# Kernel optimization log

Hardware: AMD Instinct MI355X
Metric: run time of the kernel (lower is better)

The kernel has to match this reference:

```python
import jax, jax.numpy as jnp
import numpy as np
from jax import lax

B, S, F = 64, 63, 64          # batch, window length, num_past_features
T, NF, OUT = 12, 63, 1        # pred_sequence_length, forecast feats, output_size
C, K = 32, 3                  # hidden channels, kernel size
DILS = (1, 2, 4, 8, 16)       # S = (K-1)*sum(DILS)+1 = 63 -> conv stack reduces to length 1


def setup_inputs() -> dict:
    key = jax.random.key(0)
    ks = jax.random.split(key, 8)
    sc = 0.1
    x = jax.random.normal(ks[0], (B, S, F), dtype=jnp.float32)
    x_forecasts = jax.random.normal(ks[1], (B, T, NF), dtype=jnp.float32)
    # per-feature conv stacks stored as grouped-conv weights (feature_group_count=F)
    w0 = jax.random.normal(ks[2], (F * C, 1, K), dtype=jnp.float32) * sc
    b0 = jnp.zeros((F * C,), dtype=jnp.float32)
    wmid = jax.random.normal(ks[3], (3, F * C, C, K), dtype=jnp.float32) * sc
    bmid = jnp.zeros((3, F * C), dtype=jnp.float32)
    wlast = jax.random.normal(ks[4], (F * 1, C, K), dtype=jnp.float32) * sc
    blast = jnp.zeros((F,), dtype=jnp.float32)
    linW = jax.random.normal(ks[5], (OUT, F + NF), dtype=jnp.float32) * sc
    linb = jnp.zeros((OUT,), dtype=jnp.float32)
    return dict(x=x, x_forecasts=x_forecasts, w0=w0, b0=b0, wmid=wmid,
                bmid=bmid, wlast=wlast, blast=blast, linW=linW, linb=linb)


def _dconv(h, w, d):
    # h: [B, F*Cin, L]; grouped dilated conv, one group per past feature
    return lax.conv_general_dilated(h, w, window_strides=(1,), padding='VALID',
                                    rhs_dilation=(d,),
                                    dimension_numbers=('NCH', 'OIH', 'NCH'),
                                    feature_group_count=F)


def _step(xw, xf, w0, b0, wmid, bmid, wlast, blast, linW, linb):
    # xw: [B, S, F] window; xf: [B, NF] forecast features for this step
    h = jnp.transpose(xw, (0, 2, 1))                       # [B, F, S]
    h = jax.nn.relu(_dconv(h, w0, DILS[0]) + b0[None, :, None])
    for k in range(3):
        h = jax.nn.relu(_dconv(h, wmid[k], DILS[k + 1]) + bmid[k][None, :, None])
    h = _dconv(h, wlast, DILS[4]) + blast[None, :, None]   # [B, F, 1], no final relu
    feat = jnp.concatenate([h[:, :, 0], xf], axis=1)       # [B, F+NF]
    return feat @ linW.T + linb                            # [B, OUT]


def reference(x, x_forecasts, w0, b0, wmid, bmid, wlast, blast, linW, linb):
    params = (w0, b0, wmid, bmid, wlast, blast, linW, linb)
    out0 = _step(x, x_forecasts[:, 0], *params)

    def body(carry, xs):
        xw, prev = carry
        xf_i, xf_ip1 = xs
        add = jnp.concatenate([xf_i, prev], axis=1)[:, None, :]   # [B,1,F] since NF+OUT=F
        xw = jnp.concatenate([xw[:, 1:, :], add], axis=1)          # slide window
        out = _step(xw, xf_ip1, *params)
        return (xw, out), out

    xs = (jnp.swapaxes(x_forecasts[:, :-1], 0, 1),   # [T-1, B, NF]
          jnp.swapaxes(x_forecasts[:, 1:], 0, 1))
    _, outs = lax.scan(body, (x, out0), xs)          # [T-1, B, OUT]
    return jnp.swapaxes(jnp.concatenate([out0[None], outs], axis=0), 0, 1)  # [B, T, OUT]
```

## Files before the change

### kernel.cpp

```cpp
#include <hip/hip_runtime.h>


typedef _Float16 f16;
typedef _Float16 h2 __attribute__((ext_vector_type(2)));
typedef _Float16 f16x4 __attribute__((ext_vector_type(4)));
typedef _Float16 f16x8 __attribute__((ext_vector_type(8)));
typedef float f32x16 __attribute__((ext_vector_type(16)));

#define OFF_H4    0
#define OFF_ST    49152
#define ST_L0     0
#define ST_L1     128
#define ST_L2     384
#define ST_L3     896
#define ST_STRIDE 1760
#define OFF_H40   161792
#define OFF_RECH  161856
#define OFF_PRM   166464
#define OFF_XFT   167488

#define RECH_N 9216
#define TAIL_N 59392

#define RPAD 36
#define NROW 72

__device__ __forceinline__ void stage_wrow(
    const float* __restrict__ wmid, int m, int f, int tid, f16* wrow)
{
  const float* src = wmid + m * 196608 + f * 3072 + tid * 12;
  f16* dst = wrow + (tid >> 3) * 100 + (tid & 7) * 12;
#pragma unroll
  for (int u = 0; u < 3; ++u) {
    const float4 v = *reinterpret_cast<const float4*>(src + u * 4);
    dst[u * 4 + 0] = (f16)v.x; dst[u * 4 + 1] = (f16)v.y;
    dst[u * 4 + 2] = (f16)v.z; dst[u * 4 + 3] = (f16)v.w;
  }
}

__device__ __forceinline__ void mfma_tile2(
    const f16* IN, f16* OUT, int d, int base,
    const f16* __restrict__ wrow, int lane, const float* sBias)
{
  const int lg = lane >> 5;
  const int co = lane & 31;
  const int col = base + co;

  f16x8 afr[6];
#pragma unroll
  for (int h = 0; h < 2; ++h) {
    const f16* wp = wrow + co * 100 + (h * 16 + lg * 8) * 3;
    f16x4 w4[6];
#pragma unroll
    for (int u = 0; u < 6; ++u) w4[u] = *(const f16x4*)(wp + u * 4);
#pragma unroll
    for (int t = 0; t < 3; ++t)
#pragma unroll
      for (int j = 0; j < 8; ++j) {
        const int o = 3 * j + t;
        afr[t * 2 + h][j] = w4[o >> 2][o & 3];
      }
  }

  f32x16 acc;
#pragma unroll
  for (int r = 0; r < 16; ++r)
    acc[r] = sBias[(r & 3) + 8 * (r >> 2) + 4 * lg];

#pragma unroll
  for (int t = 0; t < 3; ++t) {
#pragma unroll
    for (int h = 0; h < 2; ++h) {
      const f16* bp = IN + (col + t * d) * RPAD + h * 16 + lg * 8;
      f16x4 lo = *(const f16x4*)bp;
      f16x4 hi = *(const f16x4*)(bp + 4);
      f16x8 b = __builtin_shufflevector(lo, hi, 0, 1, 2, 3, 4, 5, 6, 7);
      acc = __builtin_amdgcn_mfma_f32_32x32x16_f16(afr[t * 2 + h], b, acc, 0, 0, 0);
    }
  }

#pragma unroll
  for (int q = 0; q < 4; ++q) {
    const int co0 = q * 8 + 4 * lg;
    f16x4 w;
#pragma unroll
    for (int e = 0; e < 4; ++e)
      w[e] = (f16)fmaxf(acc[q * 4 + e], 0.f);
    *(f16x4*)(OUT + col * RPAD + co0) = w;
  }
}

__global__ __launch_bounds__(256) void tcn_pre(
    const float* __restrict__ x, const float* __restrict__ xfc,
    const float* __restrict__ w0, const float* __restrict__ b0,
    const float* __restrict__ wmid, const float* __restrict__ bmid,
    const float* __restrict__ wlast, const float* __restrict__ blast,
    const float* __restrict__ linW, const float* __restrict__ linb,
    float* __restrict__ ws)
{
  const int blk = blockIdx.x;
  const int tid = threadIdx.x;

  if (blk >= 4096) {
    const int idx = (blk - 4096) * 256 + tid;
    if (idx < RECH_N) {
      const int e = idx & 7, lane = (idx >> 3) & 63, q = idx >> 9;
      const int i = q * 8 + e;
      const int m = i / 48, r2 = i % 48;
      const int k = r2 >> 4, ci = r2 & 15;
      const int c = lane & 31, cib = (lane >> 5) * 16;
      ((f16*)(ws + OFF_RECH))[idx] =
          (f16)wmid[m * 196608 + (2016 + c) * 96 + (cib + ci) * 3 + k];
    } else if (idx < RECH_N + 1024) {
      const int r = idx - RECH_N;
      const int e = r & 3, lane = (r >> 2) & 63, q = r >> 8;
      const int i = q * 4 + e;
      const int c = lane & 31;
      float v = 0.f;
      if (i < 3)        v = w0[(2016 + c) * 3 + i];
      else if (i == 3)  v = b0[2016 + c];
      else if (i < 7)   v = bmid[(i - 4) * 2048 + 2016 + c];
      else if (i < 10)  v = wlast[63 * 96 + c * 3 + (i - 7)];
      else if (i == 10) v = blast[63];
      else if (i == 11) v = linW[63];
      else if (i == 12) v = linb[0];
      ws[OFF_PRM + r] = v;
    } else if (idx < TAIL_N) {
      const int r = idx - (RECH_N + 1024);
      const int b = r / 768, rem = r % 768;
      const int q = rem >> 8, lane = (rem >> 2) & 63, e = rem & 3;
      const int i = q * 4 + e;
      ws[OFF_XFT + r] = (lane < 63 && i < 12) ? xfc[(b * 12 + i) * 63 + lane] : 0.f;
    }
    return;
  }

  const int b = blk >> 6;
  const int f = blk & 63;
  const bool lastf = (f == 63);
  const int lane = tid & 63;
  const int g = __builtin_amdgcn_readfirstlane(tid >> 6);

  __shared__ float sIn[80];
  __shared__ float sBias[3][32];
  __shared__ f16 actA[NROW * RPAD];
  __shared__ f16 actB[NROW * RPAD];
  __shared__ __align__(8) f16 wrow[32 * 100];

  for (int t = tid; t < 80; t += 256) {
    float v = 0.f;
    if (t < 63)                 v = x[(b * 63 + t) * 64 + f];
    else if (t < 74 && !lastf)  v = xfc[(b * 12 + (t - 63)) * 63 + f];
    sIn[t] = v;
  }
  if (tid < 96) sBias[tid >> 5][tid & 31] = bmid[(tid >> 5) * 2048 + f * 32 + (tid & 31)];
  stage_wrow(wmid, 0, f, tid, wrow);
  __syncthreads();

  {
    const float* wb  = w0 + (f * 32 + g * 8) * 3;
    const float* bbp = b0 + f * 32 + g * 8;
#pragma unroll
    for (int it = 0; it < 2; ++it) {
      const int p = lane + it * 64;
      if (p < 72) {
        const float i0 = sIn[p], i1 = sIn[p + 1], i2 = sIn[p + 2];
        f16x4 wv[2];
#pragma unroll
        for (int j = 0; j < 8; ++j) {
          float v = fmaf(wb[j * 3 + 0], i0,
                    fmaf(wb[j * 3 + 1], i1,
                    fmaf(wb[j * 3 + 2], i2, bbp[j])));
          wv[j >> 2][j & 3] = (f16)fmaxf(v, 0.f);
        }
        *(f16x4*)(actA + p * RPAD + g * 8)     = wv[0];
        *(f16x4*)(actA + p * RPAD + g * 8 + 4) = wv[1];
      }
    }
  }
  __syncthreads();

  float* st = ws + OFF_ST + b * ST_STRIDE;

  if (lastf) {
    for (int t = tid; t < 128; t += 256)
      st[ST_L0 + t] = (float)actA[(57 + (t >> 5)) * RPAD + (t & 31)];
  }
  if (g < 3) mfma_tile2(actA, actB, 2, (g == 2) ? 36 : g * 32, wrow, lane, sBias[0]);
  __syncthreads();

  stage_wrow(wmid, 1, f, tid, wrow);
  if (lastf) {
    for (int t = tid; t < 256; t += 256)
      st[ST_L1 + t] = (float)actB[(49 + (t >> 5)) * RPAD + (t & 31)];
  }
  __syncthreads();

  if (g < 2) mfma_tile2(actB, actA, 4, g * 28, wrow, lane, sBias[1]);
  __syncthreads();

  stage_wrow(wmid, 2, f, tid, wrow);
  if (lastf) {
    for (int t = tid; t < 512; t += 256)
      st[ST_L2 + t] = (float)actA[(33 + (t >> 5)) * RPAD + (t & 31)];
  }
  __syncthreads();

  if (g < 2) mfma_tile2(actA, actB, 8, g * 12, wrow, lane, sBias[2]);
  __syncthreads();

  if (lastf) {
    for (int t = tid; t < 864; t += 256)
      st[ST_L3 + t] = (float)actB[(1 + (t >> 5)) * RPAD + (t & 31)];
  }
  if (tid < 12) {
    const int p = tid;
    float acc = blast[f];
    const float* wl = wlast + f * 96;
#pragma unroll
    for (int k = 0; k < 3; ++k) {
      const int row = p + 16 * k;
#pragma unroll
      for (int ci0 = 0; ci0 < 32; ci0 += 4) {
        f16x4 av = *(const f16x4*)(actB + row * RPAD + ci0);
#pragma unroll
        for (int e = 0; e < 4; ++e)
          acc = fmaf(wl[(ci0 + e) * 3 + k], (float)av[e], acc);
      }
    }
    if (!lastf) {
      ws[OFF_H4 + b * 768 + (p >> 2) * 256 + f * 4 + (p & 3)] = acc;
    } else {
      ws[OFF_H4 + b * 768 + (p >> 2) * 256 + 63 * 4 + (p & 3)] = 0.f;
      if (p == 0) ws[OFF_H40 + b] = acc;
    }
  }
}


__device__ __forceinline__ float fd2(h2 a, h2 b, float c) {
#if __has_builtin(__builtin_amdgcn_fdot2)
  return __builtin_amdgcn_fdot2(a, b, c, false);
#else
  return fmaf((float)a[0], (float)b[0], fmaf((float)a[1], (float)b[1], c));
#endif
}

__device__ __forceinline__ float dotv(f16x8 w, f16x8 a, float acc) {
  h2 w0 = {w[0], w[1]}, a0 = {a[0], a[1]};
  h2 w1 = {w[2], w[3]}, a1 = {a[2], a[3]};
  h2 w2 = {w[4], w[5]}, a2 = {a[4], a[5]};
  h2 w3 = {w[6], w[7]}, a3 = {a[6], a[7]};
  acc = fd2(w0, a0, acc);
  acc = fd2(w1, a1, acc);
  acc = fd2(w2, a2, acc);
  acc = fd2(w3, a3, acc);
  return acc;
}

__device__ __forceinline__ f16x8 combineh(f16x8 lo, f16x8 hi) {
  f16x8 s = lo + hi;
#pragma unroll
  for (int i = 0; i < 8; ++i) s[i] = (s[i] > (f16)0.f) ? s[i] : (f16)0.f;
  return s;
}

__device__ __forceinline__ void load16f(const float* p, float* r) {
  const float4* q = reinterpret_cast<const float4*>(p);
  const float4 v0 = q[0], v1 = q[1], v2 = q[2], v3 = q[3];
  r[0]=v0.x;  r[1]=v0.y;  r[2]=v0.z;  r[3]=v0.w;
  r[4]=v1.x;  r[5]=v1.y;  r[6]=v1.z;  r[7]=v1.w;
  r[8]=v2.x;  r[9]=v2.y;  r[10]=v2.z; r[11]=v2.w;
  r[12]=v3.x; r[13]=v3.y; r[14]=v3.z; r[15]=v3.w;
}

__global__ __launch_bounds__(256, 1) void tcn_seq(
    const float* __restrict__ x,
    const float* __restrict__ linW,
    const float* __restrict__ ws, float* __restrict__ out)
{
  const int b = blockIdx.x;
  const int tid = threadIdx.x;
  const int wid = tid >> 6;
  const int lane = tid & 63;
  const int c = lane & 31;
  const int h = (lane >> 5) & 1;
  const int cib = h * 16;

  __shared__ __align__(16) f16 L0h[15 * 32];
  __shared__ __align__(16) f16 L1p[2][19 * 32];
  __shared__ __align__(16) f16 L2p[2][27 * 32];
  __shared__ __align__(16) f16 wseqh[18 * 64 * 8];
  __shared__ __align__(16) float qs[32];
  __shared__ float preArr[12];

  const float* stp = ws + OFF_ST + b * ST_STRIDE;

  if (wid == 1) {
    const f16* rech = (const f16*)(ws + OFF_RECH);
#pragma unroll
    for (int q = 0; q < 18; ++q)
      *(f16x8*)(wseqh + (q * 64 + lane) * 8) = *(const f16x8*)(rech + (q * 64 + lane) * 8);
  } else if (wid == 2) {
    for (int t = lane; t < 128; t += 64) L0h[t] = (f16)stp[ST_L0 + t];
    for (int t = lane; t < 256; t += 64) { L1p[0][t] = (f16)stp[ST_L1 + t]; L1p[1][t] = (f16)0.f; }
  } else if (wid == 3) {
    for (int t = lane; t < 512; t += 64) { L2p[0][t] = (f16)stp[ST_L2 + t]; L2p[1][t] = (f16)0.f; }
  }
  if (wid != 0) { __syncthreads(); return; }

  float prm[16];
  {
    const float* tab = ws + OFF_PRM;
#pragma unroll
    for (int q = 0; q < 4; ++q) {
      const float4 v = *reinterpret_cast<const float4*>(tab + (q * 64 + lane) * 4);
      prm[q * 4 + 0] = v.x; prm[q * 4 + 1] = v.y;
      prm[q * 4 + 2] = v.z; prm[q * 4 + 3] = v.w;
    }
  }
  const float w00 = prm[0],  w01 = prm[1],  w02 = prm[2],  b00 = prm[3];
  const float bm0 = prm[4],  bm1 = prm[5],  bm2 = prm[6];
  const float wl0c = prm[7], wl1c = prm[8], wl2c = prm[9];
  const float bl = prm[10],  lw63 = prm[11], lb0 = prm[12];

  const float xv61 = x[(b * 63 + 61) * 64 + 63];
  const float xv62 = x[(b * 63 + 62) * 64 + 63];
  const float h40v = ws[OFF_H40 + b];

  float accv[12];
  {
    float lw = 0.f, lwx = 0.f;
    if (lane < 63) { lw = linW[lane]; lwx = linW[64 + lane]; }
    float h4v[12], xv[12];
#pragma unroll
    for (int q = 0; q < 3; ++q) {
      const float4 hv  = *reinterpret_cast<const float4*>(ws + OFF_H4 + b * 768 + q * 256 + lane * 4);
      const float4 xvv = *reinterpret_cast<const float4*>(ws + OFF_XFT + b * 768 + q * 256 + lane * 4);
      h4v[q*4+0] = hv.x; h4v[q*4+1] = hv.y; h4v[q*4+2] = hv.z; h4v[q*4+3] = hv.w;
      xv[q*4+0] = xvv.x; xv[q*4+1] = xvv.y; xv[q*4+2] = xvv.z; xv[q*4+3] = xvv.w;
    }
#pragma unroll
    for (int i = 0; i < 12; ++i) accv[i] = fmaf(lw, h4v[i], lwx * xv[i]);

    if (lane < 32) {
#pragma unroll
      for (int i = 1; i < 12; ++i) {
        const float qc = fmaf(wl0c, stp[ST_L3 + (i - 1) * 32 + lane],
                              wl1c * stp[ST_L3 + (i + 15) * 32 + lane]);
        accv[i] = fmaf(lw63, qc, accv[i]);
      }
    }
#pragma unroll
    for (int r = 1; r < 64; r <<= 1) {
#pragma unroll
      for (int i = 0; i < 12; ++i) accv[i] += __shfl_xor(accv[i], r);
    }
  }
  if (lane == 0) {
#pragma unroll
    for (int i = 1; i < 12; ++i) preArr[i] = accv[i] + lb0 + lw63 * bl;
  }
  __syncthreads();

  const f16* wbase = wseqh;
  asm volatile("" : "+v"(wbase));

  const float out0 = fmaf(lw63, h40v, accv[0] + lb0);
  if (lane == 0) out[b * 12 + 0] = out0;
  float o1 = out0, o2 = xv62, o3 = xv61;

#pragma unroll 1
  for (int s = 1; s < 12; ++s) {
    const float preS = preArr[s];

    const float nL0 = fmaxf(fmaf(w00, o3, fmaf(w01, o2, fmaf(w02, o1, b00))), 0.f);
    L0h[(3 + s) * 32 + c] = (f16)nL0;

    float v1;
    {
      const f16* wp = wbase + (0 * 6 * 64 + lane) * 8;
      f16x8 W0 = *(const f16x8*)(wp);
      f16x8 W1 = *(const f16x8*)(wp + 64 * 8);
      f16x8 W2 = *(const f16x8*)(wp + 2 * 64 * 8);
      f16x8 W3 = *(const f16x8*)(wp + 3 * 64 * 8);
      f16x8 W4 = *(const f16x8*)(wp + 4 * 64 * 8);
      f16x8 W5 = *(const f16x8*)(wp + 5 * 64 * 8);
      const f16* r0p = L0h + (s - 1) * 32 + cib;
      const f16* r1p = L0h + (s + 1) * 32 + cib;
      const f16* np  = L0h + (3 + s) * 32 + cib;
      f16x8 R0a = *(const f16x8*)r0p, R0b = *(const f16x8*)(r0p + 8);
      f16x8 R1a = *(const f16x8*)r1p, R1b = *(const f16x8*)(r1p + 8);
      f16x8 Na  = *(const f16x8*)np,  Nb  = *(const f16x8*)(np + 8);
      float a0 = dotv(W0, R0a, 0.f), a1 = dotv(W1, R0b, 0.f);
      a0 = dotv(W2, R1a, a0);        a1 = dotv(W3, R1b, a1);
      a0 = dotv(W4, Na, a0);         a1 = dotv(W5, Nb, a1);
      v1 = a0 + a1 + (h == 0 ? bm0 : 0.f);
    }
    L1p[h][(7 + s) * 32 + c] = (f16)v1;

    float v2;
    {
      const f16* wp = wbase + (1 * 6 * 64 + lane) * 8;
      f16x8 W0 = *(const f16x8*)(wp);
      f16x8 W1 = *(const f16x8*)(wp + 64 * 8);
      f16x8 W2 = *(const f16x8*)(wp + 2 * 64 * 8);
      f16x8 W3 = *(const f16x8*)(wp + 3 * 64 * 8);
      f16x8 W4 = *(const f16x8*)(wp + 4 * 64 * 8);
      f16x8 W5 = *(const f16x8*)(wp + 5 * 64 * 8);
      const int i0 = (s - 1) * 32 + cib, i1 = (s + 3) * 32 + cib, in = (7 + s) * 32 + cib;
      f16x8 R0a = combineh(*(const f16x8*)(&L1p[0][i0]),     *(const f16x8*)(&L1p[1][i0]));
      f16x8 R0b = combineh(*(const f16x8*)(&L1p[0][i0 + 8]), *(const f16x8*)(&L1p[1][i0 + 8]));
      f16x8 R1a = combineh(*(const f16x8*)(&L1p[0][i1]),     *(const f16x8*)(&L1p[1][i1]));
      f16x8 R1b = combineh(*(const f16x8*)(&L1p[0][i1 + 8]), *(const f16x8*)(&L1p[1][i1 + 8]));
      f16x8 Na  = combineh(*(const f16x8*)(&L1p[0][in]),     *(const f16x8*)(&L1p[1][in]));
      f16x8 Nb  = combineh(*(const f16x8*)(&L1p[0][in + 8]), *(const f16x8*)(&L1p[1][in + 8]));
      float a0 = dotv(W0, R0a, 0.f), a1 = dotv(W1, R0b, 0.f);
      a0 = dotv(W2, R1a, a0);        a1 = dotv(W3, R1b, a1);
      a0 = dotv(W4, Na, a0);         a1 = dotv(W5, Nb, a1);
      v2 = a0 + a1 + (h == 0 ? bm1 : 0.f);
    }
    L2p[h][(15 + s) * 32 + c] = (f16)v2;

    float v3;
    {
      const f16* wp = wbase + (2 * 6 * 64 + lane) * 8;
      f16x8 W0 = *(const f16x8*)(wp);
      f16x8 W1 = *(const f16x8*)(wp + 64 * 8);
      f16x8 W2 = *(const f16x8*)(wp + 2 * 64 * 8);
      f16x8 W3 = *(const f16x8*)(wp + 3 * 64 * 8);
      f16x8 W4 = *(const f16x8*)(wp + 4 * 64 * 8);
      f16x8 W5 = *(const f16x8*)(wp + 5 * 64 * 8);
      const int i0 = (s - 1) * 32 + cib, i1 = (s + 7) * 32 + cib, in = (15 + s) * 32 + cib;
      f16x8 R0a = combineh(*(const f16x8*)(&L2p[0][i0]),     *(const f16x8*)(&L2p[1][i0]));
      f16x8 R0b = combineh(*(const f16x8*)(&L2p[0][i0 + 8]), *(const f16x8*)(&L2p[1][i0 + 8]));
      f16x8 R1a = combineh(*(const f16x8*)(&L2p[0][i1]),     *(const f16x8*)(&L2p[1][i1]));
      f16x8 R1b = combineh(*(const f16x8*)(&L2p[0][i1 + 8]), *(const f16x8*)(&L2p[1][i1 + 8]));
      f16x8 Na  = combineh(*(const f16x8*)(&L2p[0][in]),     *(const f16x8*)(&L2p[1][in]));
      f16x8 Nb  = combineh(*(const f16x8*)(&L2p[0][in + 8]), *(const f16x8*)(&L2p[1][in + 8]));
      float a0 = dotv(W0, R0a, 0.f), a1 = dotv(W1, R0b, 0.f);
      a0 = dotv(W2, R1a, a0);        a1 = dotv(W3, R1b, a1);
      a0 = dotv(W4, Na, a0);         a1 = dotv(W5, Nb, a1);
      v3 = a0 + a1 + (h == 0 ? bm2 : 0.f);
    }
    v3 += __shfl_xor(v3, 32);
    const float nL3 = fmaxf(v3, 0.f);

    if (h == 0) qs[c] = wl2c * nL3;
    float qa[16], qb[16];
    load16f(qs, qa); load16f(qs + 16, qb);
    float s0 = 0.f, s1 = 0.f, s2 = 0.f, s3 = 0.f;
#pragma unroll
    for (int i = 0; i < 16; i += 4) {
      s0 += qa[i + 0] + qb[i + 0];
      s1 += qa[i + 1] + qb[i + 1];
      s2 += qa[i + 2] + qb[i + 2];
      s3 += qa[i + 3] + qb[i + 3];
    }
    const float S = (s0 + s1) + (s2 + s3);
    const float outs = fmaf(lw63, S, preS);
    if (lane == 0) out[b * 12 + s] = outs;
    o3 = o2; o2 = o1; o1 = outs;
  }
}


extern "C" void kernel_launch(void* const* d_in, const int* in_sizes, int n_in,
                              void* d_out, int out_size, void* d_ws, size_t ws_size,
                              hipStream_t stream) {
  const float* x     = (const float*)d_in[0];
  const float* xfc   = (const float*)d_in[1];
  const float* w0    = (const float*)d_in[2];
  const float* b0    = (const float*)d_in[3];
  const float* wmid  = (const float*)d_in[4];
  const float* bmid  = (const float*)d_in[5];
  const float* wlast = (const float*)d_in[6];
  const float* blast = (const float*)d_in[7];
  const float* linW  = (const float*)d_in[8];
  const float* linb  = (const float*)d_in[9];
  float* out = (float*)d_out;
  float* ws  = (float*)d_ws;

  tcn_pre<<<4096 + 232, 256, 0, stream>>>(
      x, xfc, w0, b0, wmid, bmid, wlast, blast, linW, linb, ws);
  tcn_seq<<<64, 256, 0, stream>>>(x, linW, ws, out);
}
```

Baseline: 37.15 us.

## Process two batch elements per block in tcn_pre to reuse staged weights

Each compute block now handles two batch samples for one feature, which halves the grid from 4096 to 2048 compute blocks. The staged mid-layer weights and biases are reused across both samples, and the MFMA tiles are spread so all four waves stay busy on the layers where only two or three were active before. This cuts redundant weight loads and conversions and improves wave utilisation, at the cost of doubled LDS for activations and fewer blocks to hide latency.

```diff
diff --git a/kernel.cpp b/kernel.cpp
--- a/kernel.cpp
+++ b/kernel.cpp
@@ -21,9 +21,11 @@
 
 #define RECH_N 9216
 #define TAIL_N 59392
+#define NCOMP  2048
 
 #define RPAD 36
 #define NROW 72
+#define ASZ  (NROW * RPAD)
 
 __device__ __forceinline__ void stage_wrow(
     const float* __restrict__ wmid, int m, int f, int tid, f16* wrow)
@@ -101,8 +103,8 @@
   const int blk = blockIdx.x;
   const int tid = threadIdx.x;
 
-  if (blk >= 4096) {
-    const int idx = (blk - 4096) * 256 + tid;
+  if (blk >= NCOMP) {
+    const int idx = (blk - NCOMP) * 256 + tid;
     if (idx < RECH_N) {
       const int e = idx & 7, lane = (idx >> 3) & 63, q = idx >> 9;
       const int i = q * 8 + e;
@@ -135,23 +137,25 @@
     return;
   }
 
-  const int b = blk >> 6;
+  const int bp = blk >> 6;
   const int f = blk & 63;
   const bool lastf = (f == 63);
   const int lane = tid & 63;
   const int g = __builtin_amdgcn_readfirstlane(tid >> 6);
 
-  __shared__ float sIn[80];
+  __shared__ float sIn[2][80];
   __shared__ float sBias[3][32];
-  __shared__ f16 actA[NROW * RPAD];
-  __shared__ f16 actB[NROW * RPAD];
+  __shared__ f16 actA[2][ASZ];
+  __shared__ f16 actB[2][ASZ];
   __shared__ __align__(8) f16 wrow[32 * 100];
 
-  for (int t = tid; t < 80; t += 256) {
+  for (int t = tid; t < 160; t += 256) {
+    const int q = t / 80, tt = t % 80;
+    const int b = bp * 2 + q;
     float v = 0.f;
-    if (t < 63)                 v = x[(b * 63 + t) * 64 + f];
-    else if (t < 74 && !lastf)  v = xfc[(b * 12 + (t - 63)) * 63 + f];
-    sIn[t] = v;
+    if (tt < 63)                 v = x[(b * 63 + tt) * 64 + f];
+    else if (tt < 74 && !lastf)  v = xfc[(b * 12 + (tt - 63)) * 63 + f];
+    sIn[q][tt] = v;
   }
   if (tid < 96) sBias[tid >> 5][tid & 31] = bmid[(tid >> 5) * 2048 + f * 32 + (tid & 31)];
   stage_wrow(wmid, 0, f, tid, wrow);
@@ -161,68 +165,96 @@
     const float* wb  = w0 + (f * 32 + g * 8) * 3;
     const float* bbp = b0 + f * 32 + g * 8;
 #pragma unroll
-    for (int it = 0; it < 2; ++it) {
-      const int p = lane + it * 64;
-      if (p < 72) {
-        const float i0 = sIn[p], i1 = sIn[p + 1], i2 = sIn[p + 2];
-        f16x4 wv[2];
-#pragma unroll
-        for (int j = 0; j < 8; ++j) {
-          float v = fmaf(wb[j * 3 + 0], i0,
-                    fmaf(wb[j * 3 + 1], i1,
-                    fmaf(wb[j * 3 + 2], i2, bbp[j])));
-          wv[j >> 2][j & 3] = (f16)fmaxf(v, 0.f);
+    for (int q = 0; q < 2; ++q) {
+      const float* si = sIn[q];
+      f16* aA = actA[q];
+#pragma unroll
+      for (int it = 0; it < 2; ++it) {
+        const int p = lane + it * 64;
+        if (p < 72) {
+          const float i0 = si[p], i1 = si[p + 1], i2 = si[p + 2];
+          f16x4 wv[2];
+#pragma unroll
+          for (int j = 0; j < 8; ++j) {
+            float v = fmaf(wb[j * 3 + 0], i0,
+                      fmaf(wb[j * 3 + 1], i1,
+                      fmaf(wb[j * 3 + 2], i2, bbp[j])));
+            wv[j >> 2][j & 3] = (f16)fmaxf(v, 0.f);
+          }
+          *(f16x4*)(aA + p * RPAD + g * 8)     = wv[0];
+          *(f16x4*)(aA + p * RPAD + g * 8 + 4) = wv[1];
         }
-        *(f16x4*)(actA + p * RPAD + g * 8)     = wv[0];
-        *(f16x4*)(actA + p * RPAD + g * 8 + 4) = wv[1];
       }
     }
   }
   __syncthreads();
 
-  float* st = ws + OFF_ST + b * ST_STRIDE;
-
   if (lastf) {
-    for (int t = tid; t < 128; t += 256)
-      st[ST_L0 + t] = (float)actA[(57 + (t >> 5)) * RPAD + (t & 31)];
-  }
-  if (g < 3) mfma_tile2(actA, actB, 2, (g == 2) ? 36 : g * 32, wrow, lane, sBias[0]);
+    for (int t = tid; t < 256; t += 256) {
+      const int q = t >> 7, tt = t & 127;
+      ws[OFF_ST + (bp * 2 + q) * ST_STRIDE + ST_L0 + tt] =
+          (float)actA[q][(57 + (tt >> 5)) * RPAD + (tt & 31)];
+    }
+  }
+  {
+    int j = g;
+    {
+      const int q = j / 3, bi = j % 3;
+      mfma_tile2(actA[q], actB[q], 2, (bi == 2) ? 36 : bi * 32, wrow, lane, sBias[0]);
+    }
+    if (g < 2) {
+      j = g + 4;
+      const int q = j / 3, bi = j % 3;
+      mfma_tile2(actA[q], actB[q], 2, (bi == 2) ? 36 : bi * 32, wrow, lane, sBias[0]);
+    }
+  }
   __syncthreads();
 
   stage_wrow(wmid, 1, f, tid, wrow);
   if (lastf) {
-    for (int t = tid; t < 256; t += 256)
-      st[ST_L1 + t] = (float)actB[(49 + (t >> 5)) * RPAD + (t & 31)];
-  }
-  __syncthreads();
-
-  if (g < 2) mfma_tile2(actB, actA, 4, g * 28, wrow, lane, sBias[1]);
+    for (int t = tid; t < 512; t += 256) {
+      const int q = t >> 8, tt = t & 255;
+      ws[OFF_ST + (bp * 2 + q) * ST_STRIDE + ST_L1 + tt] =
+          (float)actB[q][(49 + (tt >> 5)) * RPAD + (tt & 31)];
+    }
+  }
+  __syncthreads();
+
+  mfma_tile2(actB[g >> 1], actA[g >> 1], 4, (g & 1) * 28, wrow, lane, sBias[1]);
   __syncthreads();
 
   stage_wrow(wmid, 2, f, tid, wrow);
   if (lastf) {
-    for (int t = tid; t < 512; t += 256)
-      st[ST_L2 + t] = (float)actA[(33 + (t >> 5)) * RPAD + (t & 31)];
-  }
-  __syncthreads();
-
-  if (g < 2) mfma_tile2(actA, actB, 8, g * 12, wrow, lane, sBias[2]);
+    for (int t = tid; t < 1024; t += 256) {
+      const int q = t >> 9, tt = t & 511;
+      ws[OFF_ST + (bp * 2 + q) * ST_STRIDE + ST_L2 + tt] =
+          (float)actA[q][(33 + (tt >> 5)) * RPAD + (tt & 31)];
+    }
+  }
+  __syncthreads();
+
+  mfma_tile2(actA[g >> 1], actB[g >> 1], 8, (g & 1) * 12, wrow, lane, sBias[2]);
   __syncthreads();
 
   if (lastf) {
-    for (int t = tid; t < 864; t += 256)
-      st[ST_L3 + t] = (float)actB[(1 + (t >> 5)) * RPAD + (t & 31)];
-  }
-  if (tid < 12) {
-    const int p = tid;
+    for (int t = tid; t < 1728; t += 256) {
+      const int q = t / 864, tt = t % 864;
+      ws[OFF_ST + (bp * 2 + q) * ST_STRIDE + ST_L3 + tt] =
+          (float)actB[q][(1 + (tt >> 5)) * RPAD + (tt & 31)];
+    }
+  }
+  if (tid < 24) {
+    const int q = tid / 12, p = tid % 12;
+    const int b = bp * 2 + q;
     float acc = blast[f];
     const float* wl = wlast + f * 96;
+    const f16* aB = actB[q];
 #pragma unroll
     for (int k = 0; k < 3; ++k) {
       const int row = p + 16 * k;
 #pragma unroll
       for (int ci0 = 0; ci0 < 32; ci0 += 4) {
-        f16x4 av = *(const f16x4*)(actB + row * RPAD + ci0);
+        f16x4 av = *(const f16x4*)(aB + row * RPAD + ci0);
 #pragma unroll
         for (int e = 0; e < 4; ++e)
           acc = fmaf(wl[(ci0 + e) * 3 + k], (float)av[e], acc);
@@ -481,7 +513,7 @@
   float* out = (float*)d_out;
   float* ws  = (float*)d_ws;
 
-  tcn_pre<<<4096 + 232, 256, 0, stream>>>(
+  tcn_pre<<<NCOMP + 232, 256, 0, stream>>>(
       x, xfc, w0, b0, wmid, bmid, wlast, blast, linW, linb, ws);
   tcn_seq<<<64, 256, 0, stream>>>(x, linW, ws, out);
 }
```

Result: faster. 36.42 us (-2.0%).
